# Kernel tuning notes

Hardware: AMD Instinct MI355X
Metric: run time of the kernel (lower is better)

## Reference

```python
import math
import jax, jax.numpy as jnp
import numpy as np

B, H_IN, W_IN = 8, 16, 16
K, STRIDE = 3, 2
IN_CAPS, OUT_CAPS = 32, 32
P_SIZE, P_DIM = 16, 4
NUM_ROUTING = 3
EPS = 1e-8
LAMBDA_0, LAMBDA_DELTA = 0.001, 0.0001
LN_2PI = math.log(2.0 * math.pi)
C_IN = IN_CAPS * (P_SIZE + 1)  # 544


def setup_inputs() -> dict:
    key = jax.random.key(0)
    k1, k2 = jax.random.split(key)
    x = jax.random.uniform(k1, (B, H_IN, W_IN, C_IN), dtype=jnp.float32)
    # weights: [K*K*in_caps, out_caps, p_dim, p_dim] (leading 1 dim of torch param dropped)
    weights = jax.random.normal(k2, (K * K * IN_CAPS, OUT_CAPS, P_DIM, P_DIM), dtype=jnp.float32)
    beta_u = jnp.full((OUT_CAPS,), 0.1, dtype=jnp.float32)
    beta_a = jnp.full((OUT_CAPS,), 0.1, dtype=jnp.float32)
    return {"input_tensor": x, "weights": weights, "beta_u": beta_u, "beta_a": beta_a}


def _kernel_tile(x):
    # x: [B, H, W, C] -> [B, K, K, oh, ow, C]
    in_h, in_w = x.shape[1:3]
    end = in_w - K + 1
    tf = np.array([[s + k for s in range(0, end, STRIDE)] for k in range(K)])  # [K, out]
    out = x[:, tf]            # [B, K, oh, W, C]
    out = out[:, :, :, tf]    # [B, K, oh, K, ow, C]
    out = jnp.transpose(out, (0, 1, 3, 2, 4, 5))  # [B, K, K, oh, ow, C]
    oh = (in_h - K + 1) // STRIDE
    ow = (in_w - K + 1) // STRIDE
    return out, oh, ow


def _matrix_transform(poses, weights):
    # poses: [N, KKL, 16] -> votes: [N, KKL, out_caps, 16]
    n = poses.shape[0]
    p4 = poses.reshape(n, -1, P_DIM, P_DIM)
    votes = jnp.einsum('nkij,kojm->nkoim', p4, weights)
    return votes.reshape(n, -1, OUT_CAPS, P_SIZE)


def _m_step(act_in, r, votes, lam, beta_u, beta_a):
    r = r * act_in                                     # [N, KKL, out]
    r = r / (r.sum(axis=2, keepdims=True) + EPS)
    r_sum = r.sum(axis=1, keepdims=True)               # [N, 1, out]
    r_prob = (r / (r_sum + EPS))[..., None]            # [N, KKL, out, 1]
    mean = (r_prob * votes).sum(axis=1, keepdims=True)  # [N, 1, out, 16]
    std = jnp.sqrt((r_prob * (votes - mean) ** 2).sum(axis=1, keepdims=True) + EPS)
    r_sum_v = r_sum.reshape(-1, OUT_CAPS, 1)
    std_v = std.reshape(-1, OUT_CAPS, P_SIZE)
    cost = (beta_u[:, None] + jnp.log(std_v)) * r_sum_v
    act_out = jax.nn.sigmoid(lam * (beta_a - cost.sum(axis=-1)))  # [N, out]
    return act_out, mean, std_v[:, None]               # std: [N, 1, out, 16]


def _e_step(mean, std, act_out, votes):
    ln_p = -(votes - mean) ** 2 / (2.0 * std ** 2) - jnp.log(std) - LN_2PI / 2.0
    ln_ap = ln_p.sum(axis=3) + jnp.log(act_out.reshape(-1, 1, OUT_CAPS))
    return jax.nn.softmax(ln_ap, axis=-1)


def _em_routing(votes, act_in, beta_u, beta_a):
    n = votes.shape[0]
    r = jnp.full(votes.shape[:-1], 1.0 / OUT_CAPS, dtype=votes.dtype)
    lam = LAMBDA_0
    mean = act_out = None
    for t in range(NUM_ROUTING):
        lam += LAMBDA_DELTA
        act_out, mean, std = _m_step(act_in, r, votes, lam, beta_u, beta_a)
        if t < NUM_ROUTING - 1:
            r = _e_step(mean, std, act_out, votes)
    return mean, act_out


def reference(input_tensor, weights, beta_u, beta_a):
    bsz = input_tensor.shape[0]
    tiled, oh, ow = _kernel_tile(input_tensor)               # [B,K,K,oh,ow,544]
    # faithful row-major reshapes (match torch .contiguous().view)
    poses = tiled[..., :-IN_CAPS].reshape(-1, K * K * IN_CAPS, P_SIZE)
    acts = tiled[..., -IN_CAPS:].reshape(-1, K * K * IN_CAPS, 1)
    votes = _matrix_transform(poses, weights)                # [N, KKL, out, 16]
    mean, act_out = _em_routing(votes, acts, beta_u, beta_a)
    poses_out = mean.reshape(bsz, oh, ow, OUT_CAPS * P_SIZE)
    act_out = act_out.reshape(bsz, oh, ow, OUT_CAPS)
    return jnp.concatenate([poses_out, act_out], axis=-1)    # [B, oh, ow, 544]
```

## Files before the change

kernel.cpp:

```cpp
#include <hip/hip_runtime.h>


namespace {

constexpr int NKK = 288;
constexpr float EPSF = 1e-8f;
constexpr float LN2PI = 1.8378770664093453f;

typedef float f32x2 __attribute__((ext_vector_type(2)));

__device__ __forceinline__ float fastrcp(float x) { return __builtin_amdgcn_rcpf(x); }
__device__ __forceinline__ f32x2 splat2(float x) { f32x2 r; r.x = x; r.y = x; return r; }
__device__ __forceinline__ f32x2 fma2(f32x2 a, f32x2 b, f32x2 c) {
    return __builtin_elementwise_fma(a, b, c);
}
__device__ __forceinline__ f32x2 lo2(float4 v) { f32x2 r; r.x = v.x; r.y = v.y; return r; }
__device__ __forceinline__ f32x2 hi2(float4 v) { f32x2 r; r.x = v.z; r.y = v.w; return r; }

template <int CTRL>
__device__ __forceinline__ float dppf(float x) {
    return __int_as_float(__builtin_amdgcn_update_dpp(
        __float_as_int(x), __float_as_int(x), CTRL, 0xF, 0xF, false));
}
__device__ __forceinline__ float swz16(float x) {
    return __int_as_float(__builtin_amdgcn_ds_swizzle(__float_as_int(x), 0x401F));
}

__device__ __forceinline__ float redmax32(float v) {
    v = fmaxf(v, dppf<0xB1>(v));
    v = fmaxf(v, dppf<0x4E>(v));
    v = fmaxf(v, dppf<0x141>(v));
    v = fmaxf(v, dppf<0x140>(v));
    v = fmaxf(v, swz16(v));
    return v;
}
__device__ __forceinline__ float redsum32(float v) {
    v += dppf<0xB1>(v);
    v += dppf<0x4E>(v);
    v += dppf<0x141>(v);
    v += dppf<0x140>(v);
    v += swz16(v);
    return v;
}

__global__ __launch_bounds__(512, 2)
void caps_em_kernel(const float* __restrict__ x,
                    const float* __restrict__ Wg,
                    const float* __restrict__ bu,
                    const float* __restrict__ ba,
                    float* __restrict__ out)
{
    __shared__ float p4[NKK * 16];
    __shared__ float cIn[NKK];
    __shared__ float scr[8 * 32 * 33];
    __shared__ float meanS[32 * 17];
    __shared__ float i2vS[32 * 17];
    __shared__ float actS[32];
    __shared__ float baseS[32];

    const int n = blockIdx.x;
    const int t = threadIdx.x;

    for (int idx = t; idx < NKK * 16; idx += 512) {
        unsigned g = (unsigned)n * 4608u + (unsigned)idx;
        unsigned c = g & 511u, rest = g >> 9;
        unsigned ow = rest % 7u; rest /= 7u;
        unsigned oh = rest % 7u; rest /= 7u;
        unsigned kw = rest % 3u; rest /= 3u;
        unsigned kh = rest % 3u;
        unsigned b  = rest / 3u;
        p4[idx] = x[((b*16u + 2u*oh + kh)*16u + 2u*ow + kw)*544u + c];
    }
    for (int idx = t; idx < NKK; idx += 512) {
        unsigned g = (unsigned)n * 288u + (unsigned)idx;
        unsigned c = g & 31u, rest = g >> 5;
        unsigned ow = rest % 7u; rest /= 7u;
        unsigned oh = rest % 7u; rest /= 7u;
        unsigned kw = rest % 3u; rest /= 3u;
        unsigned kh = rest % 3u;
        unsigned b  = rest / 3u;
        const float a = x[((b*16u + 2u*oh + kh)*16u + 2u*ow + kw)*544u + 512u + c];
        cIn[idx] = a / (a + EPSF);
    }
    __syncthreads();

    const int o  = t & 31;
    const int kc = t >> 5;
    const int oo = t >> 4;
    const int pp = t & 15;

    float lam = 1.0e-3f;

#define LOAD_W(WD, K_)                                                     \
    {                                                                      \
        const float4* wp_ = (const float4*)&Wg[((K_)*32 + o)*16];          \
        WD[0] = wp_[0]; WD[1] = wp_[1]; WD[2] = wp_[2]; WD[3] = wp_[3];    \
    }
#define LOAD_P(PD, K_)                                                     \
    {                                                                      \
        const float4* pp_ = (const float4*)&p4[(K_)*16];                   \
        PD[0] = pp_[0]; PD[1] = pp_[1]; PD[2] = pp_[2]; PD[3] = pp_[3];    \
    }

#define VOTES(PC, WC, V2)                                                  \
    _Pragma("unroll")                                                      \
    for (int i = 0; i < 4; ++i) {                                          \
        _Pragma("unroll")                                                  \
        for (int h = 0; h < 2; ++h) {                                      \
            const f32x2 w0 = (h == 0) ? lo2(WC[0]) : hi2(WC[0]);           \
            const f32x2 w1 = (h == 0) ? lo2(WC[1]) : hi2(WC[1]);           \
            const f32x2 w2 = (h == 0) ? lo2(WC[2]) : hi2(WC[2]);           \
            const f32x2 w3 = (h == 0) ? lo2(WC[3]) : hi2(WC[3]);           \
            f32x2 acc = splat2(PC[i].x) * w0;                              \
            acc = fma2(splat2(PC[i].y), w1, acc);                          \
            acc = fma2(splat2(PC[i].z), w2, acc);                          \
            acc = fma2(splat2(PC[i].w), w3, acc);                          \
            V2[i*2 + h] = acc;                                             \
        }                                                                  \
    }

#define M0_BODY(K_, PC, WC, KN_, PN, WN)                                   \
    {                                                                      \
        const float cI_ = cIn[(K_)];                                       \
        f32x2 v2[8];                                                       \
        VOTES(PC, WC, v2)                                                  \
        LOAD_P(PN, (KN_))                                                  \
        LOAD_W(WN, (KN_))                                                  \
        const float w_ = cI_ * 0.03125f;                                   \
        const f32x2 w2_ = splat2(w_);                                      \
        S0 += w_;                                                          \
        _Pragma("unroll")                                                  \
        for (int q = 0; q < 8; ++q) {                                      \
            const f32x2 wv = w2_ * v2[q];                                  \
            Svp[q] += wv;                                                  \
            Sv2p[q] = fma2(wv, v2[q], Sv2p[q]);                            \
        }                                                                  \
    }

#define E_BODY(K_, PC, WC, KN_, PN, WN)                                    \
    {                                                                      \
        const float cI_ = cIn[(K_)];                                       \
        f32x2 v2[8];                                                       \
        VOTES(PC, WC, v2)                                                  \
        LOAD_P(PN, (KN_))                                                  \
        LOAD_W(WN, (KN_))                                                  \
        f32x2 sa0 = splat2(0.f), sa1 = splat2(0.f);                        \
        _Pragma("unroll")                                                  \
        for (int q = 0; q < 8; ++q) {                                      \
            const f32x2 d = v2[q] - M2[q];                                 \
            if (q & 1) sa1 = fma2(d * d, I2[q], sa1);                      \
            else       sa0 = fma2(d * d, I2[q], sa0);                      \
        }                                                                  \
        const f32x2 sv = sa0 + sa1;                                        \
        const float lnp = base - (sv.x + sv.y);                            \
        const float e  = __expf(lnp - Mb);                                 \
        const float ss = redsum32(e);                                      \
        const float u = e * fastrcp(ss) * cI_;                             \
        S0 += u;                                                           \
        const f32x2 u2 = splat2(u);                                        \
        _Pragma("unroll")                                                  \
        for (int q = 0; q < 8; ++q) {                                      \
            const f32x2 uv = u2 * v2[q];                                   \
            Svp[q] += uv;                                                  \
            Sv2p[q] = fma2(uv, v2[q], Sv2p[q]);                            \
        }                                                                  \
    }

    for (int it = 0; it < 3; ++it) {
        lam += 1.0e-4f;

        float S0 = 0.f;
        f32x2 Svp[8], Sv2p[8];
        #pragma unroll
        for (int q = 0; q < 8; ++q) { Svp[q] = splat2(0.f); Sv2p[q] = splat2(0.f); }

        const int k0 = kc * 18;
        float4 Pa[4], Pb[4], Wa[4], Wb[4];
        LOAD_P(Pa, k0)
        LOAD_W(Wa, k0)

        if (it == 0) {
            #pragma unroll 1
            for (int kk = 0; kk < 18; kk += 2) {
                const int k = k0 + kk;
                M0_BODY(k, Pa, Wa, k + 1, Pb, Wb)
                const int kn2 = (kk == 16) ? k0 : k + 2;
                M0_BODY(k + 1, Pb, Wb, kn2, Pa, Wa)
            }
        } else {
            f32x2 M2[8], I2[8];
            #pragma unroll
            for (int q = 0; q < 8; ++q) {
                f32x2 m; m.x = meanS[o*17 + 2*q]; m.y = meanS[o*17 + 2*q + 1];
                f32x2 iv; iv.x = i2vS[o*17 + 2*q]; iv.y = i2vS[o*17 + 2*q + 1];
                M2[q] = m; I2[q] = iv;
            }
            const float base = baseS[o];
            const float Mb = redmax32(base);
            #pragma unroll 1
            for (int kk = 0; kk < 18; kk += 2) {
                const int k = k0 + kk;
                E_BODY(k, Pa, Wa, k + 1, Pb, Wb)
                const int kn2 = (kk == 16) ? k0 : k + 2;
                E_BODY(k + 1, Pb, Wb, kn2, Pa, Wa)
            }
        }

        S0 += __shfl_xor(S0, 32, 64);
        #pragma unroll
        for (int q = 0; q < 8; ++q) {
            f32x2 ta, tb;
            ta.x = __shfl_xor(Svp[q].x, 32, 64);
            ta.y = __shfl_xor(Svp[q].y, 32, 64);
            tb.x = __shfl_xor(Sv2p[q].x, 32, 64);
            tb.y = __shfl_xor(Sv2p[q].y, 32, 64);
            Svp[q] += ta;
            Sv2p[q] += tb;
        }
        if ((kc & 1) == 0) {
            float* row = &scr[((kc >> 1)*32 + o)*33];
            #pragma unroll
            for (int q = 0; q < 8; ++q) {
                row[2*q]      = Svp[q].x;  row[2*q + 1]      = Svp[q].y;
                row[16 + 2*q] = Sv2p[q].x; row[16 + 2*q + 1] = Sv2p[q].y;
            }
            row[32] = S0;
        }
        __syncthreads();

        {
            float sm = 0.f, s2 = 0.f, rs = 0.f;
            #pragma unroll
            for (int q = 0; q < 8; ++q) {
                const int b0 = (q*32 + oo)*33;
                sm += scr[b0 + pp];
                s2 += scr[b0 + 16 + pp];
                rs += scr[b0 + 32];
            }
            const float inv = 1.0f / (rs + EPSF);
            const float S1  = rs * inv;
            const float m   = sm * inv;
            float var = s2 * inv - m*m*(2.0f - S1);
            var = fmaxf(var, 0.0f) + EPSF;
            meanS[oo*17 + pp] = m;
            i2vS [oo*17 + pp] = 0.5f / var;
            scr[oo*33 + pp] = 0.5f * __logf(var);
        }
        __syncthreads();
        if (t < 32) {
            float lsum = 0.f;
            #pragma unroll
            for (int p = 0; p < 16; ++p) lsum += scr[t*33 + p];
            float rs = 0.f;
            #pragma unroll
            for (int q = 0; q < 8; ++q) rs += scr[(q*32 + t)*33 + 32];
            const float cost = (16.0f * bu[t] + lsum) * rs;
            const float ao   = 1.0f / (1.0f + __expf(-lam * (ba[t] - cost)));
            actS[t]  = ao;
            baseS[t] = -lsum - 8.0f*LN2PI + __logf(ao);
        }
        __syncthreads();
    }

#undef LOAD_P
#undef LOAD_W
#undef VOTES
#undef M0_BODY
#undef E_BODY

    for (int idx = t; idx < 544; idx += 512) {
        const float v = (idx < 512) ? meanS[(idx >> 4)*17 + (idx & 15)]
                                    : actS[idx - 512];
        out[n*544 + idx] = v;
    }
}

}

extern "C" void kernel_launch(void* const* d_in, const int* in_sizes, int n_in,
                              void* d_out, int out_size, void* d_ws, size_t ws_size,
                              hipStream_t stream) {
    (void)in_sizes; (void)n_in; (void)out_size; (void)d_ws; (void)ws_size;
    const float* x  = (const float*)d_in[0];
    const float* W  = (const float*)d_in[1];
    const float* bu = (const float*)d_in[2];
    const float* ba = (const float*)d_in[3];
    float* out = (float*)d_out;
    caps_em_kernel<<<dim3(392), dim3(512), 0, stream>>>(x, W, bu, ba, out);
}
```

Measured before the change: 126.8 us.

## Pre-transpose weights into workspace for coalesced float4 loads in routing kernel

Adds a small pre-kernel that rearranges the weight tensor into a workspace buffer so that, for each k and row j, the 32 output capsules' float4s sit next to each other. The main kernel, templated on this layout, then issues loads where adjacent lanes read adjacent float4s instead of 64-byte strided chunks. This targets the cost of the weight reads, which are repeated every routing iteration. It adds an extra kernel launch and a 590KB write/read per call, and falls back to the old path when no workspace is available.

New measurement: 123.9 us. 1.02x faster.

```diff
diff --git a/kernel.cpp b/kernel.cpp
--- a/kernel.cpp
+++ b/kernel.cpp
@@ -43,9 +43,33 @@
     return v;
 }
 
+template <bool TR>
+__device__ __forceinline__ void load_w(float4* WD, const float* __restrict__ Wg,
+                                       const float4* __restrict__ Wt4, int k, int o) {
+    if constexpr (TR) {
+        const float4* wp = Wt4 + (size_t)(k * 4) * 32 + o;
+        WD[0] = wp[0]; WD[1] = wp[32]; WD[2] = wp[64]; WD[3] = wp[96];
+    } else {
+        const float4* wp = (const float4*)&Wg[(k * 32 + o) * 16];
+        WD[0] = wp[0]; WD[1] = wp[1]; WD[2] = wp[2]; WD[3] = wp[3];
+    }
+}
+
+__global__ __launch_bounds__(256)
+void transpose_w(const float* __restrict__ Wg, float* __restrict__ Wt) {
+    const int idx = blockIdx.x * 256 + threadIdx.x;
+    const int j = idx & 3;
+    const int o = (idx >> 2) & 31;
+    const int k = idx >> 7;
+    const float4 v = ((const float4*)Wg)[idx];
+    ((float4*)Wt)[((k * 4 + j) * 32 + o)] = v;
+}
+
+template <bool TR>
 __global__ __launch_bounds__(512, 2)
 void caps_em_kernel(const float* __restrict__ x,
                     const float* __restrict__ Wg,
+                    const float4* __restrict__ Wt4,
                     const float* __restrict__ bu,
                     const float* __restrict__ ba,
                     float* __restrict__ out)
@@ -91,11 +115,6 @@
 
     float lam = 1.0e-3f;
 
-#define LOAD_W(WD, K_)                                                     \
-    {                                                                      \
-        const float4* wp_ = (const float4*)&Wg[((K_)*32 + o)*16];          \
-        WD[0] = wp_[0]; WD[1] = wp_[1]; WD[2] = wp_[2]; WD[3] = wp_[3];    \
-    }
 #define LOAD_P(PD, K_)                                                     \
     {                                                                      \
         const float4* pp_ = (const float4*)&p4[(K_)*16];                   \
@@ -125,7 +144,7 @@
         f32x2 v2[8];                                                       \
         VOTES(PC, WC, v2)                                                  \
         LOAD_P(PN, (KN_))                                                  \
-        LOAD_W(WN, (KN_))                                                  \
+        load_w<TR>(WN, Wg, Wt4, (KN_), o);                                 \
         const float w_ = cI_ * 0.03125f;                                   \
         const f32x2 w2_ = splat2(w_);                                      \
         S0 += w_;                                                          \
@@ -143,7 +162,7 @@
         f32x2 v2[8];                                                       \
         VOTES(PC, WC, v2)                                                  \
         LOAD_P(PN, (KN_))                                                  \
-        LOAD_W(WN, (KN_))                                                  \
+        load_w<TR>(WN, Wg, Wt4, (KN_), o);                                 \
         f32x2 sa0 = splat2(0.f), sa1 = splat2(0.f);                        \
         _Pragma("unroll")                                                  \
         for (int q = 0; q < 8; ++q) {                                      \
@@ -177,7 +196,7 @@
         const int k0 = kc * 18;
         float4 Pa[4], Pb[4], Wa[4], Wb[4];
         LOAD_P(Pa, k0)
-        LOAD_W(Wa, k0)
+        load_w<TR>(Wa, Wg, Wt4, k0, o);
 
         if (it == 0) {
             #pragma unroll 1
@@ -263,7 +282,6 @@
     }
 
 #undef LOAD_P
-#undef LOAD_W
 #undef VOTES
 #undef M0_BODY
 #undef E_BODY
@@ -280,11 +298,21 @@
 extern "C" void kernel_launch(void* const* d_in, const int* in_sizes, int n_in,
                               void* d_out, int out_size, void* d_ws, size_t ws_size,
                               hipStream_t stream) {
-    (void)in_sizes; (void)n_in; (void)out_size; (void)d_ws; (void)ws_size;
+    (void)in_sizes; (void)n_in; (void)out_size;
     const float* x  = (const float*)d_in[0];
     const float* W  = (const float*)d_in[1];
     const float* bu = (const float*)d_in[2];
     const float* ba = (const float*)d_in[3];
     float* out = (float*)d_out;
-    caps_em_kernel<<<dim3(392), dim3(512), 0, stream>>>(x, W, bu, ba, out);
-}
+
+    const size_t need = (size_t)NKK * 32 * 16 * sizeof(float);
+    if (d_ws != nullptr && ws_size >= need) {
+        float* Wt = (float*)d_ws;
+        transpose_w<<<dim3(144), dim3(256), 0, stream>>>(W, Wt);
+        caps_em_kernel<true><<<dim3(392), dim3(512), 0, stream>>>(
+            x, W, (const float4*)Wt, bu, ba, out);
+    } else {
+        caps_em_kernel<false><<<dim3(392), dim3(512), 0, stream>>>(
+            x, W, nullptr, bu, ba, out);
+    }
+}
```
